# Kernel tuning notes

Measured on AMD Instinct MI355X. Metric: run time of the kernel, lower is better.

## Reference

```python
import jax, jax.numpy as jnp
import numpy as np

B, S, D = 8, 2048, 128

def setup_inputs() -> dict:
    key = jax.random.key(0)
    kq, kk, kv = jax.random.split(key, 3)
    return {
        "Q": jax.random.normal(kq, (B, S, D), dtype=jnp.float32),
        "K": jax.random.normal(kk, (B, S, D), dtype=jnp.float32),
        "V": jax.random.normal(kv, (B, S, D), dtype=jnp.float32),
    }

def reference(Q, K, V):
    dim = Q.shape[-1]
    scores = jnp.einsum('bqd,bkd->bqk', Q, K) / jnp.sqrt(jnp.float32(dim))
    seq_len = Q.shape[1]
    # causal mask: -inf above the diagonal (matches torch.triu(ones*-inf, diagonal=1))
    causal = jnp.triu(jnp.full((seq_len, seq_len), -jnp.inf, dtype=scores.dtype), k=1)
    scores = scores + causal
    weights = jax.nn.softmax(scores, axis=-1)
    context = jnp.einsum('bqk,bkd->bqd', weights, V)
    return context
```

## Files before the change

kernel.cpp:

```cpp
#include <hip/hip_runtime.h>

#define B_ 8
#define S_ 2048
#define D_ 128
#define NT_ 64
#define FRAG_ 512

typedef __attribute__((ext_vector_type(4))) float f32x4;
typedef __attribute__((ext_vector_type(16))) float f32x16;
typedef __attribute__((ext_vector_type(8))) short bf16x8;
typedef __attribute__((ext_vector_type(4))) unsigned u32x4;
typedef __attribute__((ext_vector_type(2))) unsigned uint32x2;

#define MF(a, b, c) __builtin_amdgcn_mfma_f32_32x32x16_bf16(a, b, c, 0, 0, 0)

__device__ __forceinline__ short f2bf(float f) {
  union { float f; unsigned u; } x; x.f = f;
  unsigned r = x.u + 0x7FFFu + ((x.u >> 16) & 1u);
  return (short)(r >> 16);
}

__device__ __forceinline__ float exp2_hw(float x) {
  float r;
  asm("v_exp_f32 %0, %1" : "=v"(r) : "v"(x));
  return r;
}

__device__ __forceinline__ unsigned cvt_pk_bf16(float lo, float hi) {
  unsigned r;
  asm("v_cvt_pk_bf16_f32 %0, %1, %2" : "=v"(r) : "v"(lo), "v"(hi));
  return r;
}

__device__ __forceinline__ void plswap(unsigned& a, unsigned& b, int hi) {
#if __has_builtin(__builtin_amdgcn_permlane32_swap)
  uint32x2 r = __builtin_amdgcn_permlane32_swap(a, b, false, false);
  a = r[0]; b = r[1];
#else
  unsigned pa = (unsigned)__shfl_xor((int)a, 32, 64);
  unsigned pb = (unsigned)__shfl_xor((int)b, 32, 64);
  unsigned na = hi ? pb : a;
  unsigned nb = hi ? b : pa;
  a = na; b = nb;
#endif
}

__device__ __forceinline__ f32x16 zero16() {
  f32x16 v = {0.f,0.f,0.f,0.f,0.f,0.f,0.f,0.f,0.f,0.f,0.f,0.f,0.f,0.f,0.f,0.f};
  return v;
}

__global__ __launch_bounds__(256) void prep_frag(
    const float* __restrict__ Q, const float* __restrict__ K,
    const float* __restrict__ V, short* __restrict__ Qf,
    short* __restrict__ Kf, short* __restrict__ Vf) {
  __shared__ short qt[32][136], kt[32][136], vt[32][136];
  const int b  = blockIdx.x & 7;
  const int st = blockIdx.x >> 3;
  const int t  = threadIdx.x;
  const int row = t >> 3, c0 = (t & 7) * 16;
  const size_t base = ((size_t)(b * S_ + st * 32 + row)) * D_ + c0;
  const float scq = 0.12751744553939605f;

  #pragma unroll
  for (int i = 0; i < 4; ++i) {
    f32x4 q = *(const f32x4*)(Q + base + i * 4);
    f32x4 k = *(const f32x4*)(K + base + i * 4);
    f32x4 v = *(const f32x4*)(V + base + i * 4);
    #pragma unroll
    for (int j = 0; j < 4; ++j) {
      qt[row][c0 + i * 4 + j] = f2bf(q[j] * scq);
      kt[row][c0 + i * 4 + j] = f2bf(k[j]);
      vt[row][c0 + i * 4 + j] = f2bf(v[j]);
    }
  }
  __syncthreads();

  const int l = t & 63, ln = l & 31, hi = l >> 5, w = t >> 6;
  const size_t gidx = (size_t)(b * NT_ + st) * 8;
  #pragma unroll
  for (int i = 0; i < 2; ++i) {
    const int m = w * 2 + i;
    bf16x8 qv = *(const bf16x8*)&qt[ln][m * 16 + hi * 8];
    bf16x8 kv = *(const bf16x8*)&kt[ln][m * 16 + hi * 8];
    *(bf16x8*)(Qf + (gidx + m) * FRAG_ + l * 8) = qv;
    *(bf16x8*)(Kf + (gidx + m) * FRAG_ + l * 8) = kv;
    const int d4 = m >> 1, h = m & 1;
    bf16x8 vv;
    #pragma unroll
    for (int j = 0; j < 8; ++j) vv[j] = vt[h * 16 + hi * 8 + j][d4 * 32 + ln];
    *(bf16x8*)(Vf + (gidx + m) * FRAG_ + l * 8) = vv;
  }
}

__global__ __launch_bounds__(256) void fattn_fwd(
    const short* __restrict__ Qf, const short* __restrict__ Kf,
    const short* __restrict__ Vf, float* __restrict__ Og) {
  const int task = blockIdx.x;
  const int j    = task >> 3;
  const int b    = task & 7;
  const int tid  = threadIdx.x;
  const int w    = __builtin_amdgcn_readfirstlane(tid >> 6);
  const int lane = tid & 63;
  const int ln   = lane & 31;
  const int hi   = lane >> 5;
  const int lane8 = lane * 8;

  const short* Qfb = Qf + (size_t)b * (NT_ * 8 * FRAG_);
  const short* Kfb = Kf + (size_t)b * (NT_ * 8 * FRAG_);
  const short* Vfb = Vf + (size_t)b * (NT_ * 8 * FRAG_);
  float*       Ob  = Og + (size_t)b * S_ * D_;

  __shared__ float ldsO[4][4][32][33];
  __shared__ float lS[4][32], invLS[32];

#define LOADKV(KB, VA, ss) do {                                         \
    const short* kp_ = Kfb + (size_t)(ss) * (8 * FRAG_);                \
    const short* vp_ = Vfb + (size_t)(ss) * (8 * FRAG_);                \
    _Pragma("unroll")                                                   \
    for (int i_ = 0; i_ < 8; ++i_) {                                    \
      KB[i_] = *(const bf16x8*)(kp_ + i_ * FRAG_ + lane8);              \
      VA[i_] = *(const bf16x8*)(vp_ + i_ * FRAG_ + lane8);              \
    }                                                                   \
  } while (0)

#define COMPUTE(KB, VA, ss) do {                                        \
    f32x16 accA_ = zero16(), accB_ = zero16();                          \
    __builtin_amdgcn_s_setprio(1);                                      \
    _Pragma("unroll")                                                   \
    for (int dt_ = 0; dt_ < 8; dt_ += 2) {                              \
      accA_ = MF(KB[dt_],     qb[dt_],     accA_);                      \
      accB_ = MF(KB[dt_ + 1], qb[dt_ + 1], accB_);                      \
    }                                                                   \
    __builtin_amdgcn_s_setprio(0);                                      \
    f32x16 sv_ = accA_ + accB_;                                         \
    if ((ss) == tt) {                                                   \
      _Pragma("unroll")                                                 \
      for (int r_ = 0; r_ < 16; ++r_) {                                 \
        const int kl_ = (r_ & 3) + 8 * (r_ >> 2) + 4 * hi;              \
        if (kl_ > ln) sv_[r_] = -512.0f;                                \
      }                                                                 \
    }                                                                   \
    float p_[16];                                                       \
    _Pragma("unroll")                                                   \
    for (int r_ = 0; r_ < 16; ++r_) p_[r_] = exp2_hw(sv_[r_]);          \
    float ts_[8];                                                       \
    _Pragma("unroll")                                                   \
    for (int r_ = 0; r_ < 8; ++r_) ts_[r_] = p_[r_] + p_[r_ + 8];       \
    _Pragma("unroll")                                                   \
    for (int r_ = 0; r_ < 4; ++r_) ts_[r_] = ts_[r_] + ts_[r_ + 4];     \
    l_part += (ts_[0] + ts_[1]) + (ts_[2] + ts_[3]);                    \
    unsigned a0_ = cvt_pk_bf16(p_[0], p_[1]),  a1_ = cvt_pk_bf16(p_[2], p_[3]);  \
    unsigned b0_ = cvt_pk_bf16(p_[4], p_[5]),  b1_ = cvt_pk_bf16(p_[6], p_[7]);  \
    plswap(a0_, b0_, hi); plswap(a1_, b1_, hi);                         \
    unsigned c0_ = cvt_pk_bf16(p_[8], p_[9]),  c1_ = cvt_pk_bf16(p_[10], p_[11]);\
    unsigned d0_ = cvt_pk_bf16(p_[12], p_[13]), d1_ = cvt_pk_bf16(p_[14], p_[15]);\
    plswap(c0_, d0_, hi); plswap(c1_, d1_, hi);                         \
    u32x4 t0_ = {a0_, a1_, b0_, b1_};                                   \
    u32x4 t1_ = {c0_, c1_, d0_, d1_};                                   \
    bf16x8 pb0_ = __builtin_bit_cast(bf16x8, t0_);                      \
    bf16x8 pb1_ = __builtin_bit_cast(bf16x8, t1_);                      \
    __builtin_amdgcn_s_setprio(1);                                      \
    _Pragma("unroll")                                                   \
    for (int d4_ = 0; d4_ < 4; ++d4_) {                                 \
      o[d4_] = MF(VA[d4_ * 2],     pb0_, o[d4_]);                       \
      o[d4_] = MF(VA[d4_ * 2 + 1], pb1_, o[d4_]);                       \
    }                                                                   \
    __builtin_amdgcn_s_setprio(0);                                      \
  } while (0)

  #pragma unroll 1
  for (int phase = 0; phase < 2; ++phase) {
    const int tt = phase ? (63 - j) : j;
    const int q0 = tt * 32;

    bf16x8 qb[8];
    {
      const short* qfp = Qfb + (size_t)tt * (8 * FRAG_);
      #pragma unroll
      for (int dt = 0; dt < 8; ++dt)
        qb[dt] = *(const bf16x8*)(qfp + dt * FRAG_ + lane8);
    }

    f32x16 o[4];
    #pragma unroll
    for (int i = 0; i < 4; ++i) o[i] = zero16();
    float l_part = 0.f;

    if (w <= tt) {
      bf16x8 kb0[8], va0[8], kb1[8], va1[8];
      int s = w;
      LOADKV(kb0, va0, s);
      bool more1 = (s + 4 <= tt);
      if (more1) LOADKV(kb1, va1, s + 4);
      for (;;) {
        COMPUTE(kb0, va0, s);
        if (!more1) break;
        if (s + 8 <= tt) LOADKV(kb0, va0, s + 8);
        COMPUTE(kb1, va1, s + 4);
        if (s + 8 > tt) break;
        s += 8;
        more1 = (s + 4 <= tt);
        if (more1) LOADKV(kb1, va1, s + 4);
      }
    }

    float l = l_part + __shfl_xor(l_part, 32, 64);
    if (hi == 0) lS[w][ln] = l;
    #pragma unroll
    for (int d4 = 0; d4 < 4; ++d4)
      #pragma unroll
      for (int r = 0; r < 16; ++r)
        ldsO[w][d4][ln][(r & 3) + 8 * (r >> 2) + 4 * hi] = o[d4][r];
    __syncthreads();

    if (tid < 32) {
      const float L = lS[0][tid] + lS[1][tid] + lS[2][tid] + lS[3][tid];
      invLS[tid] = 1.0f / L;
    }
    __syncthreads();

    #pragma unroll
    for (int k = 0; k < 16; ++k) {
      const int e = k * 256 + tid;
      const int row = e >> 7;
      const int col = e & 127;
      float acc = 0.f;
      #pragma unroll
      for (int w2 = 0; w2 < 4; ++w2)
        acc += ldsO[w2][col >> 5][row][col & 31];
      Ob[(size_t)(q0 + row) * D_ + col] = acc * invLS[row];
    }
    __syncthreads();
  }
#undef LOADKV
#undef COMPUTE
}

extern "C" void kernel_launch(void* const* d_in, const int* in_sizes, int n_in,
                              void* d_out, int out_size, void* d_ws, size_t ws_size,
                              hipStream_t stream) {
  const float* Q = (const float*)d_in[0];
  const float* K = (const float*)d_in[1];
  const float* V = (const float*)d_in[2];
  float* O = (float*)d_out;

  short* Qf = (short*)d_ws;
  short* Kf = Qf + (size_t)B_ * S_ * D_;
  short* Vf = Kf + (size_t)B_ * S_ * D_;

  prep_frag<<<B_ * NT_, 256, 0, stream>>>(Q, K, V, Qf, Kf, Vf);
  fattn_fwd<<<B_ * 32, 256, 0, stream>>>(Qf, Kf, Vf, O);
}
```

Baseline: 34.20 us.

## Use eight waves per block for attention with two-pass LDS reduction

Doubles the block to 512 threads so eight waves split each query tile's key tiles (stride 8), and each wave prefetches the tile 16 ahead into double-buffered registers. The cross-wave output reduction reuses the existing 4-wave LDS buffer in two rounds, adding an extra barrier, and the QK MFMA chain becomes a single accumulator. The aim is more parallelism and latency hiding per tile. The costs are a longer dependent MFMA chain, higher register pressure under launch_bounds(512,2), and more synchronisation.

```diff
diff --git a/kernel.cpp b/kernel.cpp
--- a/kernel.cpp
+++ b/kernel.cpp
@@ -93,7 +93,7 @@
   }
 }
 
-__global__ __launch_bounds__(256) void fattn_fwd(
+__global__ __launch_bounds__(512, 2) void fattn_fwd(
     const short* __restrict__ Qf, const short* __restrict__ Kf,
     const short* __restrict__ Vf, float* __restrict__ Og) {
   const int task = blockIdx.x;
@@ -112,11 +112,11 @@
   float*       Ob  = Og + (size_t)b * S_ * D_;
 
   __shared__ float ldsO[4][4][32][33];
-  __shared__ float lS[4][32], invLS[32];
-
-#define LOADKV(KB, VA, ss) do {                                         \
-    const short* kp_ = Kfb + (size_t)(ss) * (8 * FRAG_);                \
-    const short* vp_ = Vfb + (size_t)(ss) * (8 * FRAG_);                \
+  __shared__ float lS[8][32], invLS[32];
+
+#define LOADT(KB, VA, SS) do {                                          \
+    const short* kp_ = Kfb + (size_t)(SS) * (8 * FRAG_);                \
+    const short* vp_ = Vfb + (size_t)(SS) * (8 * FRAG_);                \
     _Pragma("unroll")                                                   \
     for (int i_ = 0; i_ < 8; ++i_) {                                    \
       KB[i_] = *(const bf16x8*)(kp_ + i_ * FRAG_ + lane8);              \
@@ -124,17 +124,13 @@
     }                                                                   \
   } while (0)
 
-#define COMPUTE(KB, VA, ss) do {                                        \
-    f32x16 accA_ = zero16(), accB_ = zero16();                          \
+#define COMPUTE(KB, VA, SS) do {                                        \
+    f32x16 sv_ = zero16();                                              \
     __builtin_amdgcn_s_setprio(1);                                      \
     _Pragma("unroll")                                                   \
-    for (int dt_ = 0; dt_ < 8; dt_ += 2) {                              \
-      accA_ = MF(KB[dt_],     qb[dt_],     accA_);                      \
-      accB_ = MF(KB[dt_ + 1], qb[dt_ + 1], accB_);                      \
-    }                                                                   \
+    for (int dt_ = 0; dt_ < 8; ++dt_) sv_ = MF(KB[dt_], qb[dt_], sv_);  \
     __builtin_amdgcn_s_setprio(0);                                      \
-    f32x16 sv_ = accA_ + accB_;                                         \
-    if ((ss) == tt) {                                                   \
+    if ((SS) == tt) {                                                   \
       _Pragma("unroll")                                                 \
       for (int r_ = 0; r_ < 16; ++r_) {                                 \
         const int kl_ = (r_ & 3) + 8 * (r_ >> 2) + 4 * hi;              \
@@ -150,11 +146,11 @@
     _Pragma("unroll")                                                   \
     for (int r_ = 0; r_ < 4; ++r_) ts_[r_] = ts_[r_] + ts_[r_ + 4];     \
     l_part += (ts_[0] + ts_[1]) + (ts_[2] + ts_[3]);                    \
-    unsigned a0_ = cvt_pk_bf16(p_[0], p_[1]),  a1_ = cvt_pk_bf16(p_[2], p_[3]);  \
-    unsigned b0_ = cvt_pk_bf16(p_[4], p_[5]),  b1_ = cvt_pk_bf16(p_[6], p_[7]);  \
+    unsigned a0_ = cvt_pk_bf16(p_[0], p_[1]),  a1_ = cvt_pk_bf16(p_[2], p_[3]); \
+    unsigned b0_ = cvt_pk_bf16(p_[4], p_[5]),  b1_ = cvt_pk_bf16(p_[6], p_[7]); \
     plswap(a0_, b0_, hi); plswap(a1_, b1_, hi);                         \
-    unsigned c0_ = cvt_pk_bf16(p_[8], p_[9]),  c1_ = cvt_pk_bf16(p_[10], p_[11]);\
-    unsigned d0_ = cvt_pk_bf16(p_[12], p_[13]), d1_ = cvt_pk_bf16(p_[14], p_[15]);\
+    unsigned c0_ = cvt_pk_bf16(p_[8], p_[9]),  c1_ = cvt_pk_bf16(p_[10], p_[11]); \
+    unsigned d0_ = cvt_pk_bf16(p_[12], p_[13]), d1_ = cvt_pk_bf16(p_[14], p_[15]); \
     plswap(c0_, d0_, hi); plswap(c1_, d1_, hi);                         \
     u32x4 t0_ = {a0_, a1_, b0_, b1_};                                   \
     u32x4 t1_ = {c0_, c1_, d0_, d1_};                                   \
@@ -188,52 +184,80 @@
     float l_part = 0.f;
 
     if (w <= tt) {
-      bf16x8 kb0[8], va0[8], kb1[8], va1[8];
+      bf16x8 kbA[8], vaA[8], kbB[8], vaB[8];
       int s = w;
-      LOADKV(kb0, va0, s);
-      bool more1 = (s + 4 <= tt);
-      if (more1) LOADKV(kb1, va1, s + 4);
+      LOADT(kbA, vaA, s);
+      if (s + 8 <= tt) LOADT(kbB, vaB, s + 8);
+
+      #pragma unroll 1
       for (;;) {
-        COMPUTE(kb0, va0, s);
-        if (!more1) break;
-        if (s + 8 <= tt) LOADKV(kb0, va0, s + 8);
-        COMPUTE(kb1, va1, s + 4);
+        COMPUTE(kbA, vaA, s);
+        if (s + 16 <= tt) LOADT(kbA, vaA, s + 16);
         if (s + 8 > tt) break;
         s += 8;
-        more1 = (s + 4 <= tt);
-        if (more1) LOADKV(kb1, va1, s + 4);
+        COMPUTE(kbB, vaB, s);
+        if (s + 16 <= tt) LOADT(kbB, vaB, s + 16);
+        if (s + 8 > tt) break;
+        s += 8;
       }
     }
 
     float l = l_part + __shfl_xor(l_part, 32, 64);
     if (hi == 0) lS[w][ln] = l;
-    #pragma unroll
-    for (int d4 = 0; d4 < 4; ++d4)
-      #pragma unroll
-      for (int r = 0; r < 16; ++r)
-        ldsO[w][d4][ln][(r & 3) + 8 * (r >> 2) + 4 * hi] = o[d4][r];
+
+    if (w < 4) {
+      #pragma unroll
+      for (int d4 = 0; d4 < 4; ++d4)
+        #pragma unroll
+        for (int r = 0; r < 16; ++r)
+          ldsO[w][d4][ln][(r & 3) + 8 * (r >> 2) + 4 * hi] = o[d4][r];
+    }
     __syncthreads();
 
     if (tid < 32) {
-      const float L = lS[0][tid] + lS[1][tid] + lS[2][tid] + lS[3][tid];
+      float L = lS[0][tid];
+      #pragma unroll
+      for (int w2 = 1; w2 < 8; ++w2) L += lS[w2][tid];
       invLS[tid] = 1.0f / L;
     }
-    __syncthreads();
-
-    #pragma unroll
-    for (int k = 0; k < 16; ++k) {
-      const int e = k * 256 + tid;
+
+    float oacc[8];
+    #pragma unroll
+    for (int k2 = 0; k2 < 8; ++k2) {
+      const int e = k2 * 512 + tid;
       const int row = e >> 7;
       const int col = e & 127;
       float acc = 0.f;
       #pragma unroll
       for (int w2 = 0; w2 < 4; ++w2)
         acc += ldsO[w2][col >> 5][row][col & 31];
+      oacc[k2] = acc;
+    }
+    __syncthreads();
+
+    if (w >= 4) {
+      #pragma unroll
+      for (int d4 = 0; d4 < 4; ++d4)
+        #pragma unroll
+        for (int r = 0; r < 16; ++r)
+          ldsO[w - 4][d4][ln][(r & 3) + 8 * (r >> 2) + 4 * hi] = o[d4][r];
+    }
+    __syncthreads();
+
+    #pragma unroll
+    for (int k2 = 0; k2 < 8; ++k2) {
+      const int e = k2 * 512 + tid;
+      const int row = e >> 7;
+      const int col = e & 127;
+      float acc = oacc[k2];
+      #pragma unroll
+      for (int w2 = 0; w2 < 4; ++w2)
+        acc += ldsO[w2][col >> 5][row][col & 31];
       Ob[(size_t)(q0 + row) * D_ + col] = acc * invLS[row];
     }
     __syncthreads();
   }
-#undef LOADKV
+#undef LOADT
 #undef COMPUTE
 }
 
@@ -250,5 +274,5 @@
   short* Vf = Kf + (size_t)B_ * S_ * D_;
 
   prep_frag<<<B_ * NT_, 256, 0, stream>>>(Q, K, V, Qf, Kf, Vf);
-  fattn_fwd<<<B_ * 32, 256, 0, stream>>>(Qf, Kf, Vf, O);
-}
+  fattn_fwd<<<B_ * 32, 512, 0, stream>>>(Qf, Kf, Vf, O);
+}
```

Measured after the change: 48.80 us. 42.7% more time.
